# Performance work log

Measured on AMD Instinct MI355X. Metric: run time of the kernel, lower is better.

Reference implementation:

```python
import jax, jax.numpy as jnp
import numpy as np

N, E = 50000, 1600000
H, D = 2, 64            # n_heads, embed_dim (per-head out dim)
L = 3                   # n_layers
EPS = 1e-5


def setup_inputs() -> dict:
    key = jax.random.key(0)
    ks = jax.random.split(key, 16)
    s = 0.1
    return {
        "x": jax.random.normal(ks[0], (N, 64), jnp.float32),
        "src": jax.random.randint(ks[1], (E,), 0, N, jnp.int32),
        "dst": jax.random.randint(ks[2], (E,), 0, N, jnp.int32),
        "emb_w": jax.random.normal(ks[3], (64, 64), jnp.float32) * s,
        "emb_b": jnp.zeros((64,), jnp.float32),
        "fc_w": jax.random.normal(ks[4], (L, H * D, D), jnp.float32) * s,
        "attn_l": jax.random.normal(ks[5], (L, H, D), jnp.float32) * s,
        "attn_r": jax.random.normal(ks[6], (L, H, D), jnp.float32) * s,
        "gat_b": jnp.zeros((L, H * D), jnp.float32),
        "bn1_g": jnp.ones((L, H * D), jnp.float32),
        "bn1_b": jnp.zeros((L, H * D), jnp.float32),
        "ff_w1": jax.random.normal(ks[7], (L, 218, H * D), jnp.float32) * s,
        "ff_b1": jnp.zeros((L, 218), jnp.float32),
        "ff_w2": jax.random.normal(ks[8], (L, D, 218), jnp.float32) * s,
        "ff_b2": jnp.zeros((L, D), jnp.float32),
        "bn2_g": jnp.ones((L, D), jnp.float32),
        "bn2_b": jnp.zeros((L, D), jnp.float32),
        "mlp_w1": jax.random.normal(ks[9], (64, D * (L + 1)), jnp.float32) * s,
        "mlp_bn_g": jnp.ones((64,), jnp.float32),
        "mlp_bn_b": jnp.zeros((64,), jnp.float32),
        "mlp_w2": jax.random.normal(ks[10], (1, 64), jnp.float32) * s,
    }


def batch_norm(h, g, b):
    # BatchNorm1d in training mode: batch mean, biased variance
    mu = h.mean(0)
    var = ((h - mu) ** 2).mean(0)
    return g * (h - mu) * jax.lax.rsqrt(var + EPS) + b


def gat_conv(h, src, dst, fc_w, al, ar, bias):
    n = h.shape[0]
    feat = (h @ fc_w.T).reshape(n, H, D)            # [N,H,D]
    el = (feat * al).sum(-1)                        # [N,H]
    er = (feat * ar).sum(-1)                        # [N,H]
    e = jax.nn.leaky_relu(el[src] + er[dst], 0.2)   # [E,H]
    m = jax.ops.segment_max(e, dst, num_segments=n)
    ex = jnp.exp(e - m[dst])
    den = jax.ops.segment_sum(ex, dst, num_segments=n)
    alpha = ex / den[dst]                           # [E,H]
    out = jax.ops.segment_sum(alpha[:, :, None] * feat[src], dst, num_segments=n)
    return out.reshape(n, H * D) + bias             # flatten(1) + GAT bias


def reference(x, src, dst, emb_w, emb_b, fc_w, attn_l, attn_r, gat_b,
              bn1_g, bn1_b, ff_w1, ff_b1, ff_w2, ff_b2, bn2_g, bn2_b,
              mlp_w1, mlp_bn_g, mlp_bn_b, mlp_w2):
    h = x @ emb_w.T + emb_b
    xs = [h]
    for l in range(L):
        g = gat_conv(h, src, dst, fc_w[l], attn_l[l], attn_r[l], gat_b[l])
        g = batch_norm(g, bn1_g[l], bn1_b[l])
        g = jax.nn.relu(g @ ff_w1[l].T + ff_b1[l]) @ ff_w2[l].T + ff_b2[l]
        h = batch_norm(g, bn2_g[l], bn2_b[l])
        xs.append(h)
    h = jnp.concatenate(xs, axis=1)                 # JumpingKnowledge('cat')
    h = jax.nn.relu(batch_norm(h @ mlp_w1.T, mlp_bn_g, mlp_bn_b))
    return h @ mlp_w2.T                             # [N, out_dim]
```

## Files before the change

### kernel.cpp

```cpp
#include <hip/hip_runtime.h>
#include <cstdint>

#define BN_EPS 1e-5f

typedef _Float16 f16x8 __attribute__((ext_vector_type(8)));
typedef _Float16 f16x2 __attribute__((ext_vector_type(2)));
typedef float f32x4 __attribute__((ext_vector_type(4)));

__device__ __forceinline__ unsigned short f2h(float f) {
  _Float16 h = (_Float16)f;
  return *(unsigned short*)&h;
}
__device__ __forceinline__ float2 h2f2(unsigned int q) {
  f16x2 h = __builtin_bit_cast(f16x2, q);
  return make_float2((float)h.x, (float)h.y);
}

#define CHUNK 8192
#define MAXBUK 512

__global__ __launch_bounds__(256) void k_bcount(const int* __restrict__ dst, int* __restrict__ bcnt, int E) {
  __shared__ int hist[MAXBUK];
  int tid = threadIdx.x;
  int base = blockIdx.x * CHUNK;
  int cnt = min(CHUNK, E - base);
  if (cnt <= 0) return;
  for (int b = tid; b < MAXBUK; b += 256) hist[b] = 0;
  __syncthreads();
  for (int i = tid; i < cnt; i += 256) atomicAdd(&hist[dst[base + i] >> 7], 1);
  __syncthreads();
  for (int b = tid; b < MAXBUK; b += 256) {
    int c = hist[b];
    if (c > 0) atomicAdd(&bcnt[b], c);
  }
}

__global__ __launch_bounds__(512) void k_bscan(const int* __restrict__ bcnt, int* __restrict__ bcur,
                                               int* __restrict__ bbase, int nbuk) {
  __shared__ int sh[512];
  int t = threadIdx.x;
  int v = (t < nbuk) ? bcnt[t] : 0;
  sh[t] = v;
  __syncthreads();
  for (int off = 1; off < 512; off <<= 1) {
    int u = (t >= off) ? sh[t - off] : 0;
    __syncthreads();
    sh[t] += u;
    __syncthreads();
  }
  if (t < nbuk) {
    int excl = sh[t] - v;
    bcur[t] = excl;
    bbase[t] = excl;
  }
}

__global__ __launch_bounds__(256) void k_bucket(const int* __restrict__ src, const int* __restrict__ dst,
                                                int* __restrict__ bcur, unsigned int* __restrict__ pairs,
                                                int E) {
  __shared__ unsigned int ep[CHUNK];
  __shared__ int bcnt[MAXBUK];
  __shared__ int gbase[MAXBUK];
  __shared__ int rcnt[MAXBUK];
  int tid = threadIdx.x;
  int base = blockIdx.x * CHUNK;
  int cnt = min(CHUNK, E - base);
  if (cnt <= 0) return;

  for (int b = tid; b < MAXBUK; b += 256) { bcnt[b] = 0; rcnt[b] = 0; }
  __syncthreads();
  for (int i = tid; i < cnt; i += 256) {
    int d = dst[base + i];
    int s = src[base + i];
    unsigned int pk = ((unsigned)(d >> 7) << 23) | ((unsigned)(d & 127) << 16) | (unsigned)s;
    ep[i] = pk;
    atomicAdd(&bcnt[d >> 7], 1);
  }
  __syncthreads();
  for (int b = tid; b < MAXBUK; b += 256) {
    int c = bcnt[b];
    gbase[b] = (c > 0) ? atomicAdd(&bcur[b], c) : 0;
  }
  __syncthreads();
  for (int i = tid; i < cnt; i += 256) {
    unsigned int pk = ep[i];
    int bk = pk >> 23;
    int r = atomicAdd(&rcnt[bk], 1);
    pairs[gbase[bk] + r] = pk & 0x007FFFFFu;
  }
}

#define PLACE_CAP 24576

__global__ __launch_bounds__(256) void k_place(const int* __restrict__ bbase,
                                               const unsigned int* __restrict__ pairs,
                                               unsigned short* __restrict__ csr16,
                                               int* __restrict__ rowptr, int n, int nbuk, int E) {
  __shared__ unsigned short stage[PLACE_CAP];
  __shared__ int nc[128];
  __shared__ int nstart[128];
  __shared__ int nrun[128];
  int tid = threadIdx.x;
  int bk = blockIdx.x;
  int v0 = bk * 128;
  int beg = bbase[bk];
  int end = (bk + 1 < nbuk) ? bbase[bk + 1] : E;
  int cnt = end - beg;
  if (tid < 128) { nc[tid] = 0; nrun[tid] = 0; }
  __syncthreads();
  for (int i = tid; i < cnt; i += 256) atomicAdd(&nc[(pairs[beg + i] >> 16) & 127], 1);
  __syncthreads();
  if (tid < 128) nstart[tid] = nc[tid];
  __syncthreads();
  for (int off = 1; off < 128; off <<= 1) {
    int v = (tid < 128 && tid >= off) ? nstart[tid - off] : 0;
    __syncthreads();
    if (tid < 128) nstart[tid] += v;
    __syncthreads();
  }
  if (tid < 128) nstart[tid] -= nc[tid];
  __syncthreads();
  if (tid < 128 && v0 + tid < n) rowptr[v0 + tid] = beg + nstart[tid];
  if (bk == nbuk - 1 && tid == 0) rowptr[n] = E;
  if (cnt <= 0) return;
  if (cnt <= PLACE_CAP) {
    for (int i = tid; i < cnt; i += 256) {
      unsigned int p = pairs[beg + i];
      int dlow = (p >> 16) & 127;
      int r = atomicAdd(&nrun[dlow], 1);
      stage[nstart[dlow] + r] = (unsigned short)(p & 0xFFFF);
    }
    __syncthreads();
    for (int i = tid; i < cnt; i += 256) csr16[beg + i] = stage[i];
  } else {
    for (int i = tid; i < cnt; i += 256) {
      unsigned int p = pairs[beg + i];
      int dlow = (p >> 16) & 127;
      int r = atomicAdd(&nrun[dlow], 1);
      csr16[beg + nstart[dlow] + r] = (unsigned short)(p & 0xFFFF);
    }
  }
}

__global__ __launch_bounds__(256) void k_gemm(
    const void* __restrict__ Xv, int xpitch,
    const float* __restrict__ W, int wpitch,
    const float* __restrict__ bias,
    const float* __restrict__ stats, const float* __restrict__ gamma, const float* __restrict__ beta,
    float invM, void* __restrict__ Yv, int ypitch,
    int M, int KK, int COLS, int flags,
    float* __restrict__ ostats,
    const float* __restrict__ al, const float* __restrict__ ar,
    float* __restrict__ el, float* __restrict__ er) {
  __shared__ unsigned short Xs[128 * 72];
  __shared__ unsigned short Ws[64 * 72];
  __shared__ float affA[256];
  __shared__ float affB[256];

  int tid = threadIdx.x;
  int m0 = blockIdx.x * 128;
  int c0 = blockIdx.y * 64;
  const bool relu = (flags & 1) != 0;
  const bool aff = (flags & 2) != 0;
  const bool yf16 = (flags & 4) != 0;
  const bool xf16 = (flags & 8) != 0;
  const bool fstat = (flags & 16) != 0;
  const bool fattn = (flags & 32) != 0;

  if (aff) {
    if (tid < KK && tid < 256) {
      float mean = stats[tid] * invM;
      float var = stats[KK + tid] * invM - mean * mean;
      float a = gamma[tid] * rsqrtf(var + BN_EPS);
      affA[tid] = a;
      affB[tid] = beta[tid] - mean * a;
    }
    __syncthreads();
  }

  int w = tid >> 6;
  int lane = tid & 63;
  int l15 = lane & 15;
  int lhi = lane >> 4;

  f32x4 acc[2][4];
#pragma unroll
  for (int i = 0; i < 2; ++i)
#pragma unroll
    for (int j = 0; j < 4; ++j) acc[i][j] = (f32x4){0.f, 0.f, 0.f, 0.f};

  for (int kt = 0; kt < KK; kt += 64) {
    if (xf16) {
      const unsigned short* X16 = (const unsigned short*)Xv;
#pragma unroll
      for (int p = 0; p < 4; ++p) {
        int idx = p * 256 + tid;
        int r = idx >> 3;
        int k8 = (idx & 7) * 8;
        int gr = m0 + r, gk = kt + k8;
        if (gr < M && gk + 8 <= KK) {
          *(uint4*)&Xs[r * 72 + k8] = *(const uint4*)(X16 + (size_t)gr * xpitch + gk);
        } else {
#pragma unroll
          for (int j = 0; j < 8; ++j)
            Xs[r * 72 + k8 + j] =
                (gr < M && gk + j < KK) ? X16[(size_t)gr * xpitch + gk + j] : (unsigned short)0;
        }
      }
    } else {
      const float* X = (const float*)Xv;
      int rb = tid >> 4;
      int c4 = (tid & 15) * 4;
#pragma unroll
      for (int p = 0; p < 8; ++p) {
        int r = p * 16 + rb;
        int gr = m0 + r;
        int gk = kt + c4;
        float4 v = make_float4(0.f, 0.f, 0.f, 0.f);
        if (gr < M) {
          const float* px = X + (size_t)gr * xpitch;
          if (gk + 3 < KK) {
            v = *(const float4*)(px + gk);
            if (aff) {
              v.x = v.x * affA[gk] + affB[gk];
              v.y = v.y * affA[gk + 1] + affB[gk + 1];
              v.z = v.z * affA[gk + 2] + affB[gk + 2];
              v.w = v.w * affA[gk + 3] + affB[gk + 3];
            }
          } else if (gk < KK) {
            float tmp[4];
#pragma unroll
            for (int j = 0; j < 4; ++j) {
              float t = 0.f;
              if (gk + j < KK) {
                t = px[gk + j];
                if (aff) t = t * affA[gk + j] + affB[gk + j];
              }
              tmp[j] = t;
            }
            v.x = tmp[0]; v.y = tmp[1]; v.z = tmp[2]; v.w = tmp[3];
          }
        }
        ushort4 o = make_ushort4(f2h(v.x), f2h(v.y), f2h(v.z), f2h(v.w));
        *(ushort4*)&Xs[r * 72 + c4] = o;
      }
    }
    {
      int cb = tid >> 5;
      int k2 = (tid & 31) * 2;
#pragma unroll
      for (int p = 0; p < 8; ++p) {
        int c = p * 8 + cb;
        int gc = c0 + c;
        int gk = kt + k2;
        float2 v = make_float2(0.f, 0.f);
        if (gc < COLS) {
          const float* pw = W + (size_t)gc * wpitch;
          if (gk + 1 < KK) {
            v = *(const float2*)(pw + gk);
          } else if (gk < KK) {
            v.x = pw[gk];
          }
        }
        ushort2 o = make_ushort2(f2h(v.x), f2h(v.y));
        *(ushort2*)&Ws[c * 72 + k2] = o;
      }
    }
    __syncthreads();

#pragma unroll
    for (int ks = 0; ks < 64; ks += 32) {
      f16x8 a0 = *(const f16x8*)&Xs[(32 * w + l15) * 72 + ks + lhi * 8];
      f16x8 a1 = *(const f16x8*)&Xs[(32 * w + 16 + l15) * 72 + ks + lhi * 8];
#pragma unroll
      for (int ct = 0; ct < 4; ++ct) {
        f16x8 b = *(const f16x8*)&Ws[(16 * ct + l15) * 72 + ks + lhi * 8];
        acc[0][ct] = __builtin_amdgcn_mfma_f32_16x16x32_f16(a0, b, acc[0][ct], 0, 0, 0);
        acc[1][ct] = __builtin_amdgcn_mfma_f32_16x16x32_f16(a1, b, acc[1][ct], 0, 0, 0);
      }
    }
    __syncthreads();
  }

  float sArr[4] = {0.f, 0.f, 0.f, 0.f}, qArr[4] = {0.f, 0.f, 0.f, 0.f};
  float rdl[8], rdr[8];
#pragma unroll
  for (int j = 0; j < 8; ++j) { rdl[j] = 0.f; rdr[j] = 0.f; }

#pragma unroll
  for (int rt = 0; rt < 2; ++rt) {
#pragma unroll
    for (int ct = 0; ct < 4; ++ct) {
      int c = c0 + 16 * ct + l15;
      if (c >= COLS) continue;
      float bv = bias ? bias[c] : 0.f;
      float alc = fattn ? al[c] : 0.f;
      float arc = fattn ? ar[c] : 0.f;
#pragma unroll
      for (int reg = 0; reg < 4; ++reg) {
        int r = m0 + 32 * w + 16 * rt + lhi * 4 + reg;
        if (r >= M) continue;
        float vv = acc[rt][ct][reg] + bv;
        if (relu) vv = fmaxf(vv, 0.f);
        if (yf16)
          ((unsigned short*)Yv)[(size_t)r * ypitch + c] = f2h(vv);
        else
          ((float*)Yv)[(size_t)r * ypitch + c] = vv;
        if (fstat) { sArr[ct] += vv; qArr[ct] += vv * vv; }
        if (fattn) { rdl[rt * 4 + reg] += vv * alc; rdr[rt * 4 + reg] += vv * arc; }
      }
    }
  }

  if (fattn) {
#pragma unroll
    for (int j = 0; j < 8; ++j) {
      float a = rdl[j], b = rdr[j];
      a += __shfl_xor(a, 1, 64); b += __shfl_xor(b, 1, 64);
      a += __shfl_xor(a, 2, 64); b += __shfl_xor(b, 2, 64);
      a += __shfl_xor(a, 4, 64); b += __shfl_xor(b, 4, 64);
      a += __shfl_xor(a, 8, 64); b += __shfl_xor(b, 8, 64);
      rdl[j] = a; rdr[j] = b;
    }
    if (l15 == 0) {
      int hy = blockIdx.y;
#pragma unroll
      for (int j = 0; j < 8; ++j) {
        int r = m0 + 32 * w + 16 * (j >> 2) + lhi * 4 + (j & 3);
        if (r < M) {
          el[(size_t)r * 2 + hy] = rdl[j];
          er[(size_t)r * 2 + hy] = rdr[j];
        }
      }
    }
  }

  if (fstat) {
#pragma unroll
    for (int ct = 0; ct < 4; ++ct) {
      float s = sArr[ct], q = qArr[ct];
      s += __shfl_xor(s, 16, 64); q += __shfl_xor(q, 16, 64);
      s += __shfl_xor(s, 32, 64); q += __shfl_xor(q, 32, 64);
      if (lhi == 0) {
        affA[w * 64 + ct * 16 + l15] = s;
        affB[w * 64 + ct * 16 + l15] = q;
      }
    }
    __syncthreads();
    if (tid < 64) {
      float s = affA[tid] + affA[64 + tid] + affA[128 + tid] + affA[192 + tid];
      float q = affB[tid] + affB[64 + tid] + affB[128 + tid] + affB[192 + tid];
      atomicAdd(&ostats[tid], s);
      atomicAdd(&ostats[64 + tid], q);
    }
  }
}

__global__ __launch_bounds__(256) void k_agg(const int* __restrict__ rowptr,
                                             const unsigned short* __restrict__ csr16,
                                             const unsigned short* __restrict__ feat16,
                                             const float* __restrict__ el,
                                             const float* __restrict__ er, const float* __restrict__ gatb,
                                             float* __restrict__ g, int n) {
  int v = blockIdx.x * 4 + (threadIdx.x >> 6);
  if (v >= n) return;
  int lane = threadIdx.x & 63;
  int grp = lane >> 5;
  int sub = lane & 31;
  int head = sub >> 4;
  int beg = rowptr[v], end = rowptr[v + 1];
  float er0 = er[(size_t)v * 2 + 0], er1 = er[(size_t)v * 2 + 1];
  float s0 = 0.f, s1 = 0.f;
  float a0 = 0.f, a1 = 0.f, a2 = 0.f, a3 = 0.f;
  const char* fb = (const char*)feat16;
  int sub8 = sub * 8;
  for (int base = beg; base < end; base += 64) {
    int nch = min(64, end - base);
    int uoff_l = 0;
    float w0_l = 0.f, w1_l = 0.f;
    if (base + lane < end) {
      int u = csr16[base + lane];
      uoff_l = u * 256;
      float2 tt = *(const float2*)&el[(size_t)u * 2];
      float e0 = tt.x + er0, e1 = tt.y + er1;
      e0 = (e0 > 0.f) ? e0 : 0.2f * e0;
      e1 = (e1 > 0.f) ? e1 : 0.2f * e1;
      w0_l = __expf(e0);
      w1_l = __expf(e1);
      s0 += w0_l;
      s1 += w1_l;
    }
    int i = 0;
    for (; i + 16 <= nch; i += 16) {
      uint2 q[8];
#pragma unroll
      for (int p = 0; p < 8; ++p) {
        int e = i + 2 * p + grp;
        int uo = __shfl(uoff_l, e);
        q[p] = *(const uint2*)(fb + (size_t)(unsigned)uo + sub8);
      }
#pragma unroll
      for (int p = 0; p < 8; ++p) {
        int e = i + 2 * p + grp;
        float wa = __shfl(w0_l, e);
        float wb = __shfl(w1_l, e);
        float wgt = head ? wb : wa;
        float2 fx = h2f2(q[p].x);
        float2 fy = h2f2(q[p].y);
        a0 += wgt * fx.x;
        a1 += wgt * fx.y;
        a2 += wgt * fy.x;
        a3 += wgt * fy.y;
      }
    }
    for (; i + 8 <= nch; i += 8) {
      uint2 q[4];
#pragma unroll
      for (int p = 0; p < 4; ++p) {
        int e = i + 2 * p + grp;
        int uo = __shfl(uoff_l, e);
        q[p] = *(const uint2*)(fb + (size_t)(unsigned)uo + sub8);
      }
#pragma unroll
      for (int p = 0; p < 4; ++p) {
        int e = i + 2 * p + grp;
        float wa = __shfl(w0_l, e);
        float wb = __shfl(w1_l, e);
        float wgt = head ? wb : wa;
        float2 fx = h2f2(q[p].x);
        float2 fy = h2f2(q[p].y);
        a0 += wgt * fx.x;
        a1 += wgt * fx.y;
        a2 += wgt * fy.x;
        a3 += wgt * fy.y;
      }
    }
    for (; i < nch; i += 2) {
      int e = i + grp;
      int ec = min(e, nch - 1);
      int uo = __shfl(uoff_l, ec);
      float wa = __shfl(w0_l, ec);
      float wb = __shfl(w1_l, ec);
      float wgt = head ? wb : wa;
      if (e >= nch) wgt = 0.f;
      uint2 q = *(const uint2*)(fb + (size_t)(unsigned)uo + sub8);
      float2 fx = h2f2(q.x);
      float2 fy = h2f2(q.y);
      a0 += wgt * fx.x;
      a1 += wgt * fx.y;
      a2 += wgt * fy.x;
      a3 += wgt * fy.y;
    }
  }
  a0 += __shfl_xor(a0, 32, 64);
  a1 += __shfl_xor(a1, 32, 64);
  a2 += __shfl_xor(a2, 32, 64);
  a3 += __shfl_xor(a3, 32, 64);
  for (int o = 32; o > 0; o >>= 1) {
    s0 += __shfl_xor(s0, o, 64);
    s1 += __shfl_xor(s1, o, 64);
  }
  if (lane < 32) {
    float s = head ? s1 : s0;
    float inv = (end > beg) ? 1.f / s : 0.f;
    int c = 4 * sub;
    float4 o4;
    o4.x = a0 * inv + gatb[c];
    o4.y = a1 * inv + gatb[c + 1];
    o4.z = a2 * inv + gatb[c + 2];
    o4.w = a3 * inv + gatb[c + 3];
    *(float4*)&g[(size_t)v * 128 + c] = o4;
  }
}

__global__ __launch_bounds__(256) void k_colstats(const float* __restrict__ Z, int pitch, int C, int M,
                                                  float* __restrict__ stats) {
  __shared__ float ls[256];
  __shared__ float lq[256];
  int t = threadIdx.x;
  int c = t % C;
  int rpb = 256 / C;
  int r = blockIdx.x * rpb + t / C;
  int stride = gridDim.x * rpb;
  float s = 0.f, q = 0.f;
  for (; r < M; r += stride) {
    float v = Z[(size_t)r * pitch + c];
    s += v;
    q += v * v;
  }
  ls[t] = s;
  lq[t] = q;
  __syncthreads();
  if (t < C) {
    for (int i = 1; i < rpb; ++i) {
      s += ls[t + i * C];
      q += lq[t + i * C];
    }
    atomicAdd(&stats[c], s);
    atomicAdd(&stats[C + c], q);
  }
}

__global__ __launch_bounds__(256) void k_bnapply(const float* __restrict__ u, const float* __restrict__ stats,
                                                 const float* __restrict__ gam, const float* __restrict__ bet,
                                                 unsigned short* __restrict__ yout, int n, float invM) {
  int idx = blockIdx.x * 256 + threadIdx.x;
  if (idx >= n * 16) return;
  int r = idx >> 4, c4 = (idx & 15) * 4;
  float4 uu = *(const float4*)&u[(size_t)r * 64 + c4];
  float vv[4] = {uu.x, uu.y, uu.z, uu.w};
  ushort4 o;
  unsigned short* op = (unsigned short*)&o;
#pragma unroll
  for (int j = 0; j < 4; ++j) {
    int c = c4 + j;
    float mean = stats[c] * invM;
    float var = stats[64 + c] * invM - mean * mean;
    float a = gam[c] * rsqrtf(var + BN_EPS);
    float b = bet[c] - mean * a;
    op[j] = f2h(a * vv[j] + b);
  }
  *(ushort4*)&yout[(size_t)r * 256 + c4] = o;
}

__global__ __launch_bounds__(256) void k_final(const float* __restrict__ y, const float* __restrict__ stats,
                                               const float* __restrict__ gam, const float* __restrict__ bet,
                                               const float* __restrict__ w2, float* __restrict__ out, int n,
                                               float invM) {
  int v = blockIdx.x * 4 + (threadIdx.x >> 6);
  if (v >= n) return;
  int lane = threadIdx.x & 63;
  float mean = stats[lane] * invM;
  float var = stats[64 + lane] * invM - mean * mean;
  float a = gam[lane] * rsqrtf(var + BN_EPS);
  float b = bet[lane] - mean * a;
  float h = a * y[(size_t)v * 64 + lane] + b;
  h = fmaxf(h, 0.f) * w2[lane];
  for (int o = 32; o > 0; o >>= 1) h += __shfl_down(h, o, 64);
  if (lane == 0) out[v] = h;
}

extern "C" void kernel_launch(void* const* d_in, const int* in_sizes, int n_in,
                              void* d_out, int out_size, void* d_ws, size_t ws_size,
                              hipStream_t stream) {
  const float* x = (const float*)d_in[0];
  const int* src = (const int*)d_in[1];
  const int* dst = (const int*)d_in[2];
  const float* emb_w = (const float*)d_in[3];
  const float* emb_b = (const float*)d_in[4];
  const float* fc_w = (const float*)d_in[5];
  const float* attn_l = (const float*)d_in[6];
  const float* attn_r = (const float*)d_in[7];
  const float* gat_b = (const float*)d_in[8];
  const float* bn1_g = (const float*)d_in[9];
  const float* bn1_b = (const float*)d_in[10];
  const float* ff_w1 = (const float*)d_in[11];
  const float* ff_b1 = (const float*)d_in[12];
  const float* ff_w2 = (const float*)d_in[13];
  const float* ff_b2 = (const float*)d_in[14];
  const float* bn2_g = (const float*)d_in[15];
  const float* bn2_b = (const float*)d_in[16];
  const float* mlp_w1 = (const float*)d_in[17];
  const float* mlp_bn_g = (const float*)d_in[18];
  const float* mlp_bn_b = (const float*)d_in[19];
  const float* mlp_w2 = (const float*)d_in[20];
  float* out = (float*)d_out;
  (void)n_in;
  (void)out_size;

  const int n = in_sizes[0] / 64;
  const int E = in_sizes[1];
  const int NL = 3;
  const int nbuk = (n + 127) >> 7;

  char* wsb = (char*)d_ws;
  size_t off = 0;
  auto alloc = [&](size_t bytes) {
    size_t o = off;
    off = (off + bytes + 255) & ~(size_t)255;
    return o;
  };
  size_t o_bcnt = alloc((size_t)512 * 4);
  size_t o_stats = alloc(1280 * 4);
  size_t zero_bytes = off;
  size_t o_rowptr = alloc((size_t)(n + 1) * 4);
  size_t o_bcur = alloc((size_t)512 * 4);
  size_t o_bbase = alloc((size_t)512 * 4);
  size_t o_csr = alloc((size_t)E * 2);
  size_t o_pairs = alloc((size_t)E * 4);
  size_t o_feat = alloc((size_t)n * 64 * 4);
  size_t o_g = alloc((size_t)n * 128 * 4);
  size_t o_t = alloc((size_t)n * 224 * 2 + 256);
  size_t o_xs = alloc((size_t)n * 256 * 2);
  size_t o_el = alloc((size_t)n * 2 * 4);
  size_t o_er = alloc((size_t)n * 2 * 4);
  if (off > ws_size) return;

  int* bcnt = (int*)(wsb + o_bcnt);
  float* stats = (float*)(wsb + o_stats);
  int* rowptr = (int*)(wsb + o_rowptr);
  int* bcur = (int*)(wsb + o_bcur);
  int* bbase = (int*)(wsb + o_bbase);
  unsigned short* csr16 = (unsigned short*)(wsb + o_csr);
  unsigned int* pairs = (unsigned int*)(wsb + o_pairs);
  unsigned short* feat16 = (unsigned short*)(wsb + o_feat);
  float* g = (float*)(wsb + o_g);
  unsigned short* t16 = (unsigned short*)(wsb + o_t);
  unsigned short* xs16 = (unsigned short*)(wsb + o_xs);
  float* el = (float*)(wsb + o_el);
  float* er = (float*)(wsb + o_er);
  float* u = (float*)(wsb + o_feat);

  hipMemsetAsync(d_ws, 0, zero_bytes, stream);

  int gchunk = (E + CHUNK - 1) / CHUNK;
  k_bcount<<<gchunk, 256, 0, stream>>>(dst, bcnt, E);
  k_bscan<<<1, 512, 0, stream>>>(bcnt, bcur, bbase, nbuk);
  k_bucket<<<gchunk, 256, 0, stream>>>(src, dst, bcur, pairs, E);
  k_place<<<nbuk, 256, 0, stream>>>(bbase, pairs, csr16, rowptr, n, nbuk, E);

  int gm = (n + 127) / 128;
  float invM = 1.f / (float)n;

  k_gemm<<<dim3(gm, 1), 256, 0, stream>>>(x, 64, emb_w, 64, emb_b, nullptr, nullptr, nullptr, invM,
                                          xs16, 256, n, 64, 64, 4,
                                          nullptr, nullptr, nullptr, nullptr, nullptr);

  for (int l = 0; l < NL; ++l) {
    float* sbn1 = stats + l * 384;
    float* sbn2 = stats + l * 384 + 256;
    k_gemm<<<dim3(gm, 2), 256, 0, stream>>>(xs16 + 64 * l, 256, fc_w + (size_t)l * 128 * 64, 64,
                                            nullptr, nullptr, nullptr, nullptr, invM,
                                            feat16, 128, n, 64, 128, 4 | 8 | 32,
                                            nullptr, attn_l + l * 128, attn_r + l * 128, el, er);
    k_agg<<<(n + 3) / 4, 256, 0, stream>>>(rowptr, csr16, feat16, el, er, gat_b + l * 128, g, n);
    k_colstats<<<512, 256, 0, stream>>>(g, 128, 128, n, sbn1);
    k_gemm<<<dim3(gm, 4), 256, 0, stream>>>(g, 128, ff_w1 + (size_t)l * 218 * 128, 128, ff_b1 + l * 218,
                                            sbn1, bn1_g + l * 128, bn1_b + l * 128, invM,
                                            t16, 224, n, 128, 218, 1 | 2 | 4,
                                            nullptr, nullptr, nullptr, nullptr, nullptr);
    k_gemm<<<dim3(gm, 1), 256, 0, stream>>>(t16, 224, ff_w2 + (size_t)l * 64 * 218, 218, ff_b2 + l * 64,
                                            nullptr, nullptr, nullptr, invM,
                                            u, 64, n, 218, 64, 8 | 16,
                                            sbn2, nullptr, nullptr, nullptr, nullptr);
    k_bnapply<<<(n * 16 + 255) / 256, 256, 0, stream>>>(u, sbn2, bn2_g + l * 64, bn2_b + l * 64,
                                                        xs16 + 64 * (l + 1), n, invM);
  }

  float* smlp = stats + 1152;
  k_gemm<<<dim3(gm, 1), 256, 0, stream>>>(xs16, 256, mlp_w1, 256, nullptr, nullptr, nullptr, nullptr, invM,
                                          u, 64, n, 256, 64, 8 | 16,
                                          smlp, nullptr, nullptr, nullptr, nullptr);
  k_final<<<(n + 3) / 4, 256, 0, stream>>>(u, smlp, mlp_bn_g, mlp_bn_b, mlp_w2, out, n, invM);
}
```

Before: 772.4 us.

## Store GAT output in fp16, fold BN1 into FF weights, pre-convert weights

The aggregation output g is now written as fp16 instead of fp32, which halves its write traffic and the reads by colstats and the FF1 GEMM. The BN1 affine transform is folded into ff_w1 and its bias by a small per-layer kernel, so the FF1 GEMM reads plain fp16 input with no per-element affine step. All weights are converted to fp16 once (ff_w2 padded to 224 columns) so GEMM tiles load them with vectorized 8-byte reads. The cost is extra small launches and fp16 rounding of the pre-BN activations and of the folded weights.

```diff
diff --git a/kernel.cpp b/kernel.cpp
--- a/kernel.cpp
+++ b/kernel.cpp
@@ -142,9 +142,60 @@
   }
 }
 
+__global__ __launch_bounds__(256) void k_cvtw(
+    const float* __restrict__ emb, const float* __restrict__ fc,
+    const float* __restrict__ w2, const float* __restrict__ mlp,
+    unsigned short* __restrict__ o_emb, unsigned short* __restrict__ o_fc,
+    unsigned short* __restrict__ o_w2, unsigned short* __restrict__ o_mlp,
+    int n_emb, int n_fc, int n_w2rows, int n_mlp) {
+  int idx = blockIdx.x * 256 + threadIdx.x;
+  if (idx < n_emb) { o_emb[idx] = f2h(emb[idx]); return; }
+  idx -= n_emb;
+  if (idx < n_fc) { o_fc[idx] = f2h(fc[idx]); return; }
+  idx -= n_fc;
+  int w2tot = n_w2rows * 224;
+  if (idx < w2tot) {
+    int r = idx / 224, c = idx - r * 224;
+    o_w2[idx] = f2h((c < 218) ? w2[r * 218 + c] : 0.f);
+    return;
+  }
+  idx -= w2tot;
+  if (idx < n_mlp) o_mlp[idx] = f2h(mlp[idx]);
+}
+
+__global__ __launch_bounds__(256) void k_foldw1(const float* __restrict__ W1, const float* __restrict__ b1,
+                                                const float* __restrict__ stats, const float* __restrict__ gam,
+                                                const float* __restrict__ bet, float invM,
+                                                unsigned short* __restrict__ W16, float* __restrict__ b1p,
+                                                int rows, int K) {
+  __shared__ float aA[128];
+  __shared__ float aB[128];
+  int tid = threadIdx.x;
+  if (tid < K) {
+    float mean = stats[tid] * invM;
+    float var = stats[K + tid] * invM - mean * mean;
+    float a = gam[tid] * rsqrtf(var + BN_EPS);
+    aA[tid] = a;
+    aB[tid] = bet[tid] - mean * a;
+  }
+  __syncthreads();
+  int w = tid >> 6, lane = tid & 63;
+  int i = blockIdx.x * 4 + w;
+  if (i >= rows) return;
+  const float* wr = W1 + (size_t)i * K;
+  float dot = 0.f;
+  for (int k = lane; k < K; k += 64) {
+    float wv = wr[k];
+    W16[(size_t)i * K + k] = f2h(wv * aA[k]);
+    dot += wv * aB[k];
+  }
+  for (int o = 32; o > 0; o >>= 1) dot += __shfl_down(dot, o, 64);
+  if (lane == 0) b1p[i] = b1[i] + dot;
+}
+
 __global__ __launch_bounds__(256) void k_gemm(
     const void* __restrict__ Xv, int xpitch,
-    const float* __restrict__ W, int wpitch,
+    const void* __restrict__ Wv, int wpitch,
     const float* __restrict__ bias,
     const float* __restrict__ stats, const float* __restrict__ gamma, const float* __restrict__ beta,
     float invM, void* __restrict__ Yv, int ypitch,
@@ -166,6 +217,7 @@
   const bool xf16 = (flags & 8) != 0;
   const bool fstat = (flags & 16) != 0;
   const bool fattn = (flags & 32) != 0;
+  const bool wf16 = (flags & 64) != 0;
 
   if (aff) {
     if (tid < KK && tid < 256) {
@@ -245,7 +297,22 @@
         *(ushort4*)&Xs[r * 72 + c4] = o;
       }
     }
-    {
+    if (wf16) {
+      const unsigned short* W16 = (const unsigned short*)Wv;
+#pragma unroll
+      for (int p = 0; p < 4; ++p) {
+        int idx = p * 256 + tid;
+        int c = idx >> 4;
+        int k4 = (idx & 15) * 4;
+        int gc = c0 + c, gk = kt + k4;
+        uint2 val = make_uint2(0u, 0u);
+        if (gc < COLS && gk + 4 <= wpitch) {
+          val = *(const uint2*)(W16 + (size_t)gc * wpitch + gk);
+        }
+        *(uint2*)&Ws[c * 72 + k4] = val;
+      }
+    } else {
+      const float* W = (const float*)Wv;
       int cb = tid >> 5;
       int k2 = (tid & 31) * 2;
 #pragma unroll
@@ -361,7 +428,7 @@
                                              const unsigned short* __restrict__ feat16,
                                              const float* __restrict__ el,
                                              const float* __restrict__ er, const float* __restrict__ gatb,
-                                             float* __restrict__ g, int n) {
+                                             unsigned short* __restrict__ g16, int n) {
   int v = blockIdx.x * 4 + (threadIdx.x >> 6);
   if (v >= n) return;
   int lane = threadIdx.x & 63;
@@ -464,17 +531,17 @@
     float s = head ? s1 : s0;
     float inv = (end > beg) ? 1.f / s : 0.f;
     int c = 4 * sub;
-    float4 o4;
-    o4.x = a0 * inv + gatb[c];
-    o4.y = a1 * inv + gatb[c + 1];
-    o4.z = a2 * inv + gatb[c + 2];
-    o4.w = a3 * inv + gatb[c + 3];
-    *(float4*)&g[(size_t)v * 128 + c] = o4;
-  }
-}
-
-__global__ __launch_bounds__(256) void k_colstats(const float* __restrict__ Z, int pitch, int C, int M,
-                                                  float* __restrict__ stats) {
+    ushort4 o4;
+    o4.x = f2h(a0 * inv + gatb[c]);
+    o4.y = f2h(a1 * inv + gatb[c + 1]);
+    o4.z = f2h(a2 * inv + gatb[c + 2]);
+    o4.w = f2h(a3 * inv + gatb[c + 3]);
+    *(ushort4*)&g16[(size_t)v * 128 + c] = o4;
+  }
+}
+
+__global__ __launch_bounds__(256) void k_colstats16(const unsigned short* __restrict__ Z, int pitch,
+                                                    int C, int M, float* __restrict__ stats) {
   __shared__ float ls[256];
   __shared__ float lq[256];
   int t = threadIdx.x;
@@ -483,8 +550,9 @@
   int r = blockIdx.x * rpb + t / C;
   int stride = gridDim.x * rpb;
   float s = 0.f, q = 0.f;
+  const _Float16* Zh = (const _Float16*)Z;
   for (; r < M; r += stride) {
-    float v = Z[(size_t)r * pitch + c];
+    float v = (float)Zh[(size_t)r * pitch + c];
     s += v;
     q += v * v;
   }
@@ -589,11 +657,21 @@
   size_t o_csr = alloc((size_t)E * 2);
   size_t o_pairs = alloc((size_t)E * 4);
   size_t o_feat = alloc((size_t)n * 64 * 4);
-  size_t o_g = alloc((size_t)n * 128 * 4);
+  size_t o_g = alloc((size_t)n * 128 * 2);
   size_t o_t = alloc((size_t)n * 224 * 2 + 256);
   size_t o_xs = alloc((size_t)n * 256 * 2);
   size_t o_el = alloc((size_t)n * 2 * 4);
   size_t o_er = alloc((size_t)n * 2 * 4);
+  const int n_emb = 64 * 64;
+  const int n_fc = NL * 128 * 64;
+  const int n_w2rows = NL * 64;
+  const int n_mlp = 64 * 256;
+  size_t o_embw = alloc((size_t)n_emb * 2);
+  size_t o_fcw = alloc((size_t)n_fc * 2);
+  size_t o_w2w = alloc((size_t)n_w2rows * 224 * 2);
+  size_t o_mlpw = alloc((size_t)n_mlp * 2);
+  size_t o_w1f = alloc((size_t)218 * 128 * 2);
+  size_t o_b1p = alloc((size_t)224 * 4);
   if (off > ws_size) return;
 
   int* bcnt = (int*)(wsb + o_bcnt);
@@ -604,11 +682,17 @@
   unsigned short* csr16 = (unsigned short*)(wsb + o_csr);
   unsigned int* pairs = (unsigned int*)(wsb + o_pairs);
   unsigned short* feat16 = (unsigned short*)(wsb + o_feat);
-  float* g = (float*)(wsb + o_g);
+  unsigned short* g16 = (unsigned short*)(wsb + o_g);
   unsigned short* t16 = (unsigned short*)(wsb + o_t);
   unsigned short* xs16 = (unsigned short*)(wsb + o_xs);
   float* el = (float*)(wsb + o_el);
   float* er = (float*)(wsb + o_er);
+  unsigned short* embw16 = (unsigned short*)(wsb + o_embw);
+  unsigned short* fcw16 = (unsigned short*)(wsb + o_fcw);
+  unsigned short* w2w16 = (unsigned short*)(wsb + o_w2w);
+  unsigned short* mlpw16 = (unsigned short*)(wsb + o_mlpw);
+  unsigned short* w1f16 = (unsigned short*)(wsb + o_w1f);
+  float* b1p = (float*)(wsb + o_b1p);
   float* u = (float*)(wsb + o_feat);
 
   hipMemsetAsync(d_ws, 0, zero_bytes, stream);
@@ -619,37 +703,45 @@
   k_bucket<<<gchunk, 256, 0, stream>>>(src, dst, bcur, pairs, E);
   k_place<<<nbuk, 256, 0, stream>>>(bbase, pairs, csr16, rowptr, n, nbuk, E);
 
+  int cvt_total = n_emb + n_fc + n_w2rows * 224 + n_mlp;
+  k_cvtw<<<(cvt_total + 255) / 256, 256, 0, stream>>>(emb_w, fc_w, ff_w2, mlp_w1,
+                                                      embw16, fcw16, w2w16, mlpw16,
+                                                      n_emb, n_fc, n_w2rows, n_mlp);
+
   int gm = (n + 127) / 128;
   float invM = 1.f / (float)n;
 
-  k_gemm<<<dim3(gm, 1), 256, 0, stream>>>(x, 64, emb_w, 64, emb_b, nullptr, nullptr, nullptr, invM,
-                                          xs16, 256, n, 64, 64, 4,
+  k_gemm<<<dim3(gm, 1), 256, 0, stream>>>(x, 64, embw16, 64, emb_b, nullptr, nullptr, nullptr, invM,
+                                          xs16, 256, n, 64, 64, 4 | 64,
                                           nullptr, nullptr, nullptr, nullptr, nullptr);
 
   for (int l = 0; l < NL; ++l) {
     float* sbn1 = stats + l * 384;
     float* sbn2 = stats + l * 384 + 256;
-    k_gemm<<<dim3(gm, 2), 256, 0, stream>>>(xs16 + 64 * l, 256, fc_w + (size_t)l * 128 * 64, 64,
+    k_gemm<<<dim3(gm, 2), 256, 0, stream>>>(xs16 + 64 * l, 256, fcw16 + (size_t)l * 128 * 64, 64,
                                             nullptr, nullptr, nullptr, nullptr, invM,
-                                            feat16, 128, n, 64, 128, 4 | 8 | 32,
+                                            feat16, 128, n, 64, 128, 4 | 8 | 32 | 64,
                                             nullptr, attn_l + l * 128, attn_r + l * 128, el, er);
-    k_agg<<<(n + 3) / 4, 256, 0, stream>>>(rowptr, csr16, feat16, el, er, gat_b + l * 128, g, n);
-    k_colstats<<<512, 256, 0, stream>>>(g, 128, 128, n, sbn1);
-    k_gemm<<<dim3(gm, 4), 256, 0, stream>>>(g, 128, ff_w1 + (size_t)l * 218 * 128, 128, ff_b1 + l * 218,
-                                            sbn1, bn1_g + l * 128, bn1_b + l * 128, invM,
-                                            t16, 224, n, 128, 218, 1 | 2 | 4,
+    k_agg<<<(n + 3) / 4, 256, 0, stream>>>(rowptr, csr16, feat16, el, er, gat_b + l * 128, g16, n);
+    k_colstats16<<<512, 256, 0, stream>>>(g16, 128, 128, n, sbn1);
+    k_foldw1<<<(218 + 3) / 4, 256, 0, stream>>>(ff_w1 + (size_t)l * 218 * 128, ff_b1 + l * 218,
+                                                sbn1, bn1_g + l * 128, bn1_b + l * 128, invM,
+                                                w1f16, b1p, 218, 128);
+    k_gemm<<<dim3(gm, 4), 256, 0, stream>>>(g16, 128, w1f16, 128, b1p,
+                                            nullptr, nullptr, nullptr, invM,
+                                            t16, 224, n, 128, 218, 1 | 4 | 8 | 64,
                                             nullptr, nullptr, nullptr, nullptr, nullptr);
-    k_gemm<<<dim3(gm, 1), 256, 0, stream>>>(t16, 224, ff_w2 + (size_t)l * 64 * 218, 218, ff_b2 + l * 64,
+    k_gemm<<<dim3(gm, 1), 256, 0, stream>>>(t16, 224, w2w16 + (size_t)l * 64 * 224, 224, ff_b2 + l * 64,
                                             nullptr, nullptr, nullptr, invM,
-                                            u, 64, n, 218, 64, 8 | 16,
+                                            u, 64, n, 218, 64, 8 | 16 | 64,
                                             sbn2, nullptr, nullptr, nullptr, nullptr);
     k_bnapply<<<(n * 16 + 255) / 256, 256, 0, stream>>>(u, sbn2, bn2_g + l * 64, bn2_b + l * 64,
                                                         xs16 + 64 * (l + 1), n, invM);
   }
 
   float* smlp = stats + 1152;
-  k_gemm<<<dim3(gm, 1), 256, 0, stream>>>(xs16, 256, mlp_w1, 256, nullptr, nullptr, nullptr, nullptr, invM,
-                                          u, 64, n, 256, 64, 8 | 16,
+  k_gemm<<<dim3(gm, 1), 256, 0, stream>>>(xs16, 256, mlpw16, 256, nullptr, nullptr, nullptr, nullptr, invM,
+                                          u, 64, n, 256, 64, 8 | 16 | 64,
                                           smlp, nullptr, nullptr, nullptr, nullptr);
   k_final<<<(n + 3) / 4, 256, 0, stream>>>(u, smlp, mlp_bn_g, mlp_bn_b, mlp_w2, out, n, invM);
 }
```

Measured after the change: 665.0 us, median of 2. -13.9%, faster.
